# Performance work log

Hardware: AMD Instinct MI355X
Metric: run time of the kernel (lower is better)

Reference implementation:

```python
import jax, jax.numpy as jnp
import numpy as np

H = 1024
A = H // 2
B = 32
S = 1024
T = 1024


def setup_inputs() -> dict:
    key = jax.random.key(0)
    ks = jax.random.split(key, 16)
    sc = 0.02
    inp = {
        "hidden": jax.random.normal(ks[0], (1, B, H), jnp.float32),
        "encoder_hiddens": jax.random.normal(ks[1], (S, B, H), jnp.float32),
        "h0_s": jax.random.normal(ks[2], (T, B, H), jnp.float32),
        "ax": jax.random.uniform(ks[3], (B, S, 1), jnp.float32),
        # weights: torch Linear(in,out,bias=False) -> W has shape [out,in], y = x @ W.T
        "W1": jax.random.normal(ks[4], (A, H), jnp.float32) * sc,
        "W2": jax.random.normal(ks[5], (A, H), jnp.float32) * sc,
        "W3": jax.random.normal(ks[6], (A, 1), jnp.float32) * sc,
        "W4": jax.random.normal(ks[7], (1, 3 * A), jnp.float32) * sc,
        "W5": jax.random.normal(ks[8], (A, H), jnp.float32) * sc,
        "W6": jax.random.normal(ks[9], (A, H), jnp.float32) * sc,
        "W7": jax.random.normal(ks[10], (A, H), jnp.float32) * sc,
        "W8": jax.random.normal(ks[11], (1, 3 * A), jnp.float32) * sc,
        "W9": jax.random.normal(ks[12], (H, H), jnp.float32) * sc,
        "W10": jax.random.normal(ks[13], (H, H), jnp.float32) * sc,
        "W11": jax.random.normal(ks[14], (1, 2 * H), jnp.float32) * sc,
    }
    return inp


def reference(hidden, encoder_hiddens, h0_s, ax,
              W1, W2, W3, W4, W5, W6, W7, W8, W9, W10, W11):
    h = hidden[0]  # [B,H], hidden.squeeze(0)

    # ---- encoder (x) attention with coverage, vectorized over S ----
    wx = jnp.einsum('sbh,ah->sba', encoder_hiddens, W1)          # [S,B,A]
    wxy = h @ W2.T                                               # [B,A]
    # Linear3 on ax[:, j] ([B,1]): outer product with W3 column
    wxr = ax[:, :, 0][:, :, None] * W3[:, 0][None, None, :]       # [B,S,A]
    wxr = jnp.transpose(wxr, (1, 0, 2))                           # [S,B,A]
    cat_x = jnp.tanh(jnp.concatenate(
        [wx, jnp.broadcast_to(wxy, (S,) + wxy.shape), wxr], axis=-1))  # [S,B,3A]
    exi = jnp.einsum('sbc,oc->bso', cat_x, W4)                    # [B,S,1]
    axi = jax.nn.softmax(exi, axis=1)                             # [B,S,1]
    cxi = jnp.einsum('bs,sbh->bh', axi[:, :, 0], encoder_hiddens)  # [B,H]
    ax_new = ax + axi

    # ---- decoder-history (t) attention, vectorized over T ----
    wt = jnp.einsum('tbh,ah->tba', h0_s, W5)                      # [T,B,A]
    wtx = cxi @ W6.T                                              # [B,A]
    wty = h @ W7.T                                                # [B,A]
    Tn = h0_s.shape[0]
    cat_t = jnp.tanh(jnp.concatenate(
        [wt,
         jnp.broadcast_to(wtx, (Tn,) + wtx.shape),
         jnp.broadcast_to(wty, (Tn,) + wty.shape)], axis=-1))     # [T,B,3A]
    eti = jnp.einsum('tbc,oc->bto', cat_t, W8)                    # [B,T,1]
    ati = jax.nn.softmax(eti, axis=1)
    cti = jnp.einsum('bt,tbh->bh', ati[:, :, 0], h0_s)            # [B,H]

    # ---- gated fusion ----
    gxi = jnp.tanh(cxi @ W9.T)
    gti = jnp.tanh(cti @ W10.T)
    zi = jax.nn.sigmoid(jnp.concatenate([cxi, cti], axis=1) @ W11.T)  # [B,1]
    ci = zi * gxi + (1.0 - zi) * gti                              # [B,H]
    return ci, ax_new
```

## Files before the change

### kernel.cpp

```cpp
#include <hip/hip_runtime.h>
#include <hip/hip_bf16.h>

#define HH 1024
#define AA 512
#define BB 32
#define SS 1024
#define TN 1024
#define M_ENC (SS*BB)
#define M_TOT ((SS+TN)*BB)
#define NCH 8

typedef __attribute__((ext_vector_type(8))) short short8;
typedef __attribute__((ext_vector_type(4))) float f4;

union bfu { __hip_bfloat16 h; unsigned short u; };
__device__ __forceinline__ unsigned short f2b(float x) {
  bfu t; t.h = __float2bfloat16(x); return t.u;
}
__device__ __forceinline__ float tanh_fast(float x) {
  float e = __expf(2.f * x);
  return 1.f - 2.f / (e + 1.f);
}

__global__ void wprep(const float* __restrict__ W, unsigned short* __restrict__ Wc) {
  const int t = blockIdx.x * 256 + threadIdx.x;
  const int lane = t & 63;
  const int rg = (t >> 6) & 31;
  const int kb = t >> 11;
  const int row = rg * 16 + (lane & 15);
  const int k = kb * 32 + ((lane >> 4) << 3);
  const float* src = W + (size_t)row * HH + k;
  f4 v0 = *(const f4*)(src);
  f4 v1 = *(const f4*)(src + 4);
  short8 o;
  o[0] = f2b(v0[0]); o[1] = f2b(v0[1]); o[2] = f2b(v0[2]); o[3] = f2b(v0[3]);
  o[4] = f2b(v1[0]); o[5] = f2b(v1[1]); o[6] = f2b(v1[2]); o[7] = f2b(v1[3]);
  *(short8*)(Wc + (size_t)t * 8) = o;
}

__global__ __launch_bounds__(1024, 4)
void e1_gemm(const float* __restrict__ enc, const float* __restrict__ h0,
             const unsigned short* __restrict__ W1c, const unsigned short* __restrict__ W5c,
             const float* __restrict__ W4, const float* __restrict__ W8,
             float* __restrict__ e1) {
  const int wg   = blockIdx.x;
  const int tid  = threadIdx.x;
  const int lane = tid & 63;
  const int wave = tid >> 6;
  const int rowg = wave >> 3;
  const int colg = wave & 7;
  const int l15  = lane & 15;
  const int lg   = lane >> 4;

  const bool is_enc = (wg * 128) < M_ENC;
  const float* __restrict__ Xg = is_enc ? enc : h0;
  const unsigned short* __restrict__ Wc = is_enc ? W1c : W5c;
  const float* __restrict__ Vg = is_enc ? W4 : W8;
  const int row0 = is_enc ? wg * 128 : wg * 128 - M_ENC;

  __shared__ char lds_raw[2 * 49152 + 4096];
  float* lred = (float*)(lds_raw + 2 * 49152);

  float vvv[4];
#pragma unroll
  for (int cf = 0; cf < 4; ++cf) vvv[cf] = Vg[colg * 64 + cf * 16 + l15];

  f4 acc[4][4];
#pragma unroll
  for (int i = 0; i < 4; ++i)
#pragma unroll
    for (int j = 0; j < 4; ++j) acc[i][j] = (f4){0.f, 0.f, 0.f, 0.f};

#define STAGE(buf, kb_) do {                                                  \
    const int kbase_ = (kb_) * 32;                                            \
    const int arow_ = tid >> 3;                                               \
    const int sl_ = tid & 7;                                                  \
    const int sg_ = sl_ ^ (arow_ & 7);                                        \
    const float* gA_ = Xg + (size_t)(row0 + arow_) * HH + kbase_ + sg_ * 4;   \
    char* lA_ = lds_raw + (buf) * 49152 + tid * 16;                           \
    __builtin_amdgcn_global_load_lds(                                         \
        (const __attribute__((address_space(1))) void*)gA_,                   \
        (__attribute__((address_space(3))) void*)lA_, 16, 0, 0);              \
    _Pragma("unroll")                                                         \
    for (int p_ = 0; p_ < 2; ++p_) {                                          \
      const int idx_ = p_ * 1024 + tid;                                       \
      const char* gB_ = (const char*)Wc + (size_t)(kb_) * 32768 + idx_ * 16;  \
      char* lB_ = lds_raw + (buf) * 49152 + 16384 + idx_ * 16;                \
      __builtin_amdgcn_global_load_lds(                                       \
          (const __attribute__((address_space(1))) void*)gB_,                 \
          (__attribute__((address_space(3))) void*)lB_, 16, 0, 0);            \
    }                                                                         \
  } while (0)

  STAGE(0, 0);
  __syncthreads();

  int cur = 0;
#pragma unroll 1
  for (int kb = 0; kb < 32; ++kb) {
    if (kb < 31) STAGE(cur ^ 1, kb + 1);

    const char* Ab = lds_raw + cur * 49152;
    const char* Bb = Ab + 16384;

    short8 bfr[4];
#pragma unroll
    for (int cf = 0; cf < 4; ++cf)
      bfr[cf] = *(const short8*)(Bb + (((colg * 4 + cf) * 64 + lane) * 16));

#pragma unroll
    for (int rt = 0; rt < 4; ++rt) {
      const int row = rowg * 64 + rt * 16 + l15;
      const int x = row & 7;
      f4 a0 = *(const f4*)(Ab + row * 128 + (((lg * 2)     ^ x) * 16));
      f4 a1 = *(const f4*)(Ab + row * 128 + (((lg * 2 + 1) ^ x) * 16));
      short8 af;
      af[0] = f2b(a0[0]); af[1] = f2b(a0[1]); af[2] = f2b(a0[2]); af[3] = f2b(a0[3]);
      af[4] = f2b(a1[0]); af[5] = f2b(a1[1]); af[6] = f2b(a1[2]); af[7] = f2b(a1[3]);
#pragma unroll
      for (int cf = 0; cf < 4; ++cf)
        acc[rt][cf] = __builtin_amdgcn_mfma_f32_16x16x32_bf16(af, bfr[cf], acc[rt][cf], 0, 0, 0);
    }
    __syncthreads();
    cur ^= 1;
  }
#undef STAGE

#pragma unroll
  for (int rt = 0; rt < 4; ++rt) {
    float ps[4] = {0.f, 0.f, 0.f, 0.f};
#pragma unroll
    for (int cf = 0; cf < 4; ++cf) {
      const float w = vvv[cf];
#pragma unroll
      for (int r = 0; r < 4; ++r) ps[r] += w * tanh_fast(acc[rt][cf][r]);
    }
#pragma unroll
    for (int r = 0; r < 4; ++r) {
#pragma unroll
      for (int off = 1; off < 16; off <<= 1) ps[r] += __shfl_xor(ps[r], off);
    }
    if (l15 == 0) {
#pragma unroll
      for (int r = 0; r < 4; ++r)
        lred[colg * 128 + rowg * 64 + rt * 16 + lg * 4 + r] = ps[r];
    }
  }
  __syncthreads();
  if (tid < 128) {
    float s = 0.f;
#pragma unroll
    for (int c = 0; c < 8; ++c) s += lred[c * 128 + tid];
    e1[(size_t)wg * 128 + tid] = s;
  }
}

__global__ void exf_kernel(const float* __restrict__ e1, const float* __restrict__ ax,
                           const float* __restrict__ W3, const float* __restrict__ W4,
                           float* __restrict__ exf) {
  __shared__ float w3s[AA], w4r[AA];
  const int tid = threadIdx.x;
  for (int i = tid; i < AA; i += 256) { w3s[i] = W3[i]; w4r[i] = W4[2 * AA + i]; }
  __syncthreads();
  const int b = blockIdx.x >> 2;
  const int s = (blockIdx.x & 3) * 256 + tid;
  const float x = ax[b * SS + s];
  float er = 0.f;
#pragma unroll 8
  for (int a = 0; a < AA; ++a) er += w4r[a] * tanh_fast(x * w3s[a]);
  exf[b * SS + s] = e1[s * BB + b] + er;
}

__global__ void softmax_bs(const float* __restrict__ ein, const float* __restrict__ ax,
                           float* __restrict__ wout, float* __restrict__ axnew) {
  const int b = blockIdx.x, tid = threadIdx.x;
  __shared__ float red[256];
  float loc[4];
  float m = -1e30f;
#pragma unroll
  for (int i = 0; i < 4; ++i) { loc[i] = ein[b * SS + i * 256 + tid]; m = fmaxf(m, loc[i]); }
  red[tid] = m; __syncthreads();
  for (int off = 128; off > 0; off >>= 1) {
    if (tid < off) red[tid] = fmaxf(red[tid], red[tid + off]);
    __syncthreads();
  }
  m = red[0]; __syncthreads();
  float sum = 0.f;
#pragma unroll
  for (int i = 0; i < 4; ++i) { loc[i] = __expf(loc[i] - m); sum += loc[i]; }
  red[tid] = sum; __syncthreads();
  for (int off = 128; off > 0; off >>= 1) {
    if (tid < off) red[tid] += red[tid + off];
    __syncthreads();
  }
  const float inv = 1.f / red[0];
#pragma unroll
  for (int i = 0; i < 4; ++i) {
    const int s = i * 256 + tid;
    const float a_ = loc[i] * inv;
    wout[b * SS + s] = a_;
    axnew[b * SS + s] = ax[b * SS + s] + a_;
  }
}

__global__ void softmax_tb(const float* __restrict__ ein, float* __restrict__ wout) {
  const int b = blockIdx.x, tid = threadIdx.x;
  __shared__ float red[256];
  float loc[4];
  float m = -1e30f;
#pragma unroll
  for (int i = 0; i < 4; ++i) { loc[i] = ein[(i * 256 + tid) * BB + b]; m = fmaxf(m, loc[i]); }
  red[tid] = m; __syncthreads();
  for (int off = 128; off > 0; off >>= 1) {
    if (tid < off) red[tid] = fmaxf(red[tid], red[tid + off]);
    __syncthreads();
  }
  m = red[0]; __syncthreads();
  float sum = 0.f;
#pragma unroll
  for (int i = 0; i < 4; ++i) { loc[i] = __expf(loc[i] - m); sum += loc[i]; }
  red[tid] = sum; __syncthreads();
  for (int off = 128; off > 0; off >>= 1) {
    if (tid < off) red[tid] += red[tid + off];
    __syncthreads();
  }
  const float inv = 1.f / red[0];
#pragma unroll
  for (int i = 0; i < 4; ++i) wout[b * TN + (i * 256 + tid)] = loc[i] * inv;
}

__global__ void wpart(const float* __restrict__ X, const float* __restrict__ w,
                      float* __restrict__ part) {
  const int b = blockIdx.x / NCH, ch = blockIdx.x % NCH;
  const int tid = threadIdx.x;
  __shared__ float ws[SS / NCH];
  if (tid < SS / NCH) ws[tid] = w[b * SS + ch * (SS / NCH) + tid];
  __syncthreads();
  f4 acc = (f4){0.f, 0.f, 0.f, 0.f};
  const float* base = X + ((size_t)(ch * (SS / NCH)) * BB + b) * HH + tid * 4;
  for (int i = 0; i < SS / NCH; ++i) {
    f4 x = *(const f4*)(base + (size_t)i * BB * HH);
    acc += ws[i] * x;
  }
  *(f4*)&part[((size_t)(b * NCH + ch)) * HH + tid * 4] = acc;
}

__global__ void wreduce(const float* __restrict__ part, float* __restrict__ out) {
  const int idx = blockIdx.x * 256 + threadIdx.x;
  const int b = idx / HH, h = idx % HH;
  float s = 0.f;
#pragma unroll
  for (int ch = 0; ch < NCH; ++ch) s += part[((size_t)(b * NCH + ch)) * HH + h];
  out[idx] = s;
}

__global__ void zi_kernel(const float* __restrict__ cxi, const float* __restrict__ cti,
                          const float* __restrict__ W11, float* __restrict__ zi) {
  const int b = blockIdx.x, tid = threadIdx.x;
  float s = 0.f;
  for (int i = tid; i < HH; i += 256) s += cxi[b * HH + i] * W11[i] + cti[b * HH + i] * W11[HH + i];
  __shared__ float red[4];
  for (int off = 32; off > 0; off >>= 1) s += __shfl_down(s, off);
  if ((tid & 63) == 0) red[tid >> 6] = s;
  __syncthreads();
  if (tid == 0) {
    float t = red[0] + red[1] + red[2] + red[3];
    zi[b] = 1.f / (1.f + __expf(-t));
  }
}

__global__ void ci_kernel(const float* __restrict__ cxi, const float* __restrict__ cti,
                          const float* __restrict__ W9, const float* __restrict__ W10,
                          const float* __restrict__ zi, float* __restrict__ out_ci) {
  const int b = blockIdx.x >> 2, hb = blockIdx.x & 3, tid = threadIdx.x;
  const int h = hb * 256 + tid;
  __shared__ float cx[HH], ct[HH];
  for (int i = tid; i < HH; i += 256) { cx[i] = cxi[b * HH + i]; ct[i] = cti[b * HH + i]; }
  __syncthreads();
  const float* __restrict__ w9r  = W9  + (size_t)h * HH;
  const float* __restrict__ w10r = W10 + (size_t)h * HH;
  float gx = 0.f, gt = 0.f;
  for (int k = 0; k < HH; k += 4) {
    f4 a = *(const f4*)(w9r + k);
    f4 c = *(const f4*)(w10r + k);
    gx += cx[k] * a[0] + cx[k + 1] * a[1] + cx[k + 2] * a[2] + cx[k + 3] * a[3];
    gt += ct[k] * c[0] + ct[k + 1] * c[1] + ct[k + 2] * c[2] + ct[k + 3] * c[3];
  }
  const float z = zi[b];
  out_ci[b * HH + h] = z * tanhf(gx) + (1.f - z) * tanhf(gt);
}

extern "C" void kernel_launch(void* const* d_in, const int* in_sizes, int n_in,
                              void* d_out, int out_size, void* d_ws, size_t ws_size,
                              hipStream_t stream) {
  const float* enc = (const float*)d_in[1];
  const float* h0  = (const float*)d_in[2];
  const float* ax  = (const float*)d_in[3];
  const float* W1  = (const float*)d_in[4];
  const float* W3  = (const float*)d_in[6];
  const float* W4  = (const float*)d_in[7];
  const float* W5  = (const float*)d_in[8];
  const float* W8  = (const float*)d_in[11];
  const float* W9  = (const float*)d_in[12];
  const float* W10 = (const float*)d_in[13];
  const float* W11 = (const float*)d_in[14];
  float* out = (float*)d_out;

  float* w = (float*)d_ws;
  unsigned short* W1c = (unsigned short*)w;
  unsigned short* W5c = (unsigned short*)(w + 262144);
  float* partx = w;
  float* partt = w + 262144;
  float* e1    = w + 524288;
  float* exf   = w + 589824;
  float* axi   = w + 622592;
  float* ati   = w + 655360;
  float* cxi   = w + 688128;
  float* cti   = w + 720896;
  float* zi    = w + 753664;

  wprep<<<256, 256, 0, stream>>>(W1, W1c);
  wprep<<<256, 256, 0, stream>>>(W5, W5c);
  e1_gemm<<<M_TOT / 128, 1024, 0, stream>>>(enc, h0, W1c, W5c, W4, W8, e1);
  exf_kernel<<<BB * 4, 256, 0, stream>>>(e1, ax, W3, W4, exf);
  softmax_bs<<<BB, 256, 0, stream>>>(exf, ax, axi, out + BB * HH);
  softmax_tb<<<BB, 256, 0, stream>>>(e1 + M_ENC, ati);
  wpart<<<BB * NCH, 256, 0, stream>>>(enc, axi, partx);
  wpart<<<BB * NCH, 256, 0, stream>>>(h0, ati, partt);
  wreduce<<<BB * HH / 256, 256, 0, stream>>>(partx, cxi);
  wreduce<<<BB * HH / 256, 256, 0, stream>>>(partt, cti);
  zi_kernel<<<BB, 256, 0, stream>>>(cxi, cti, W11, zi);
  ci_kernel<<<BB * 4, 256, 0, stream>>>(cxi, cti, W9, W10, zi, out);
}
```

Baseline: 256.4 us.

## Convert A tile to bf16 once on load instead of per MFMA read

The GEMM's fp32 A tile used to be copied straight into LDS with global_load_lds, and every wave converted it to bf16 on each read. Now half the threads load A into registers, convert it to bf16 once, and write a swizzled bf16 tile into LDS after the MFMA loop. This halves the A footprint in LDS (from 96KB+ down to 80KB total) and removes redundant conversions. The trade-off is register-staged loads instead of async direct-to-LDS copies. The weighted-sum loop in wpart is also unrolled by 4.

```diff
diff --git a/kernel.cpp b/kernel.cpp
--- a/kernel.cpp
+++ b/kernel.cpp
@@ -58,8 +58,8 @@
   const float* __restrict__ Vg = is_enc ? W4 : W8;
   const int row0 = is_enc ? wg * 128 : wg * 128 - M_ENC;
 
-  __shared__ char lds_raw[2 * 49152 + 4096];
-  float* lred = (float*)(lds_raw + 2 * 49152);
+  __shared__ char lds_raw[2 * 40960];
+  float* lred = (float*)lds_raw;
 
   float vvv[4];
 #pragma unroll
@@ -71,60 +71,75 @@
 #pragma unroll
     for (int j = 0; j < 4; ++j) acc[i][j] = (f4){0.f, 0.f, 0.f, 0.f};
 
-#define STAGE(buf, kb_) do {                                                  \
-    const int kbase_ = (kb_) * 32;                                            \
-    const int arow_ = tid >> 3;                                               \
-    const int sl_ = tid & 7;                                                  \
-    const int sg_ = sl_ ^ (arow_ & 7);                                        \
-    const float* gA_ = Xg + (size_t)(row0 + arow_) * HH + kbase_ + sg_ * 4;   \
-    char* lA_ = lds_raw + (buf) * 49152 + tid * 16;                           \
-    __builtin_amdgcn_global_load_lds(                                         \
-        (const __attribute__((address_space(1))) void*)gA_,                   \
-        (__attribute__((address_space(3))) void*)lA_, 16, 0, 0);              \
+  const int arow  = tid >> 2;
+  const int kslot = tid & 3;
+  const int acol  = kslot ^ ((arow >> 1) & 3);
+  const float* aSrc = Xg + (size_t)(row0 + arow) * HH + kslot * 8;
+  const int aDst = arow * 64 + acol * 16;
+
+  const int aRd = (rowg * 64 + l15) * 64 + ((lg ^ ((l15 >> 1) & 3)) << 4);
+  const int bRd = colg * 4096 + lane * 16;
+
+#define BGLL(buf, kb_) do {                                                   \
     _Pragma("unroll")                                                         \
     for (int p_ = 0; p_ < 2; ++p_) {                                          \
       const int idx_ = p_ * 1024 + tid;                                       \
       const char* gB_ = (const char*)Wc + (size_t)(kb_) * 32768 + idx_ * 16;  \
-      char* lB_ = lds_raw + (buf) * 49152 + 16384 + idx_ * 16;                \
+      char* lB_ = lds_raw + (buf) * 40960 + 8192 + idx_ * 16;                 \
       __builtin_amdgcn_global_load_lds(                                       \
           (const __attribute__((address_space(1))) void*)gB_,                 \
           (__attribute__((address_space(3))) void*)lB_, 16, 0, 0);            \
     }                                                                         \
   } while (0)
 
-  STAGE(0, 0);
+#define AWRITE(buf, v0_, v1_) do {                                            \
+    short8 o_;                                                                \
+    o_[0] = f2b(v0_[0]); o_[1] = f2b(v0_[1]);                                 \
+    o_[2] = f2b(v0_[2]); o_[3] = f2b(v0_[3]);                                 \
+    o_[4] = f2b(v1_[0]); o_[5] = f2b(v1_[1]);                                 \
+    o_[6] = f2b(v1_[2]); o_[7] = f2b(v1_[3]);                                 \
+    *(short8*)(lds_raw + (buf) * 40960 + aDst) = o_;                          \
+  } while (0)
+
+  f4 a0n, a1n;
+  if (tid < 512) { a0n = *(const f4*)(aSrc); a1n = *(const f4*)(aSrc + 4); }
+  BGLL(0, 0);
+  if (tid < 512) AWRITE(0, a0n, a1n);
   __syncthreads();
 
   int cur = 0;
 #pragma unroll 1
   for (int kb = 0; kb < 32; ++kb) {
-    if (kb < 31) STAGE(cur ^ 1, kb + 1);
-
-    const char* Ab = lds_raw + cur * 49152;
-    const char* Bb = Ab + 16384;
+    if (kb < 31) {
+      if (tid < 512) {
+        a0n = *(const f4*)(aSrc + (kb + 1) * 32);
+        a1n = *(const f4*)(aSrc + (kb + 1) * 32 + 4);
+      }
+      BGLL(cur ^ 1, kb + 1);
+    }
+
+    const char* Ab = lds_raw + cur * 40960;
+    const char* Bb = Ab + 8192;
 
     short8 bfr[4];
 #pragma unroll
     for (int cf = 0; cf < 4; ++cf)
-      bfr[cf] = *(const short8*)(Bb + (((colg * 4 + cf) * 64 + lane) * 16));
+      bfr[cf] = *(const short8*)(Bb + bRd + cf * 1024);
 
 #pragma unroll
     for (int rt = 0; rt < 4; ++rt) {
-      const int row = rowg * 64 + rt * 16 + l15;
-      const int x = row & 7;
-      f4 a0 = *(const f4*)(Ab + row * 128 + (((lg * 2)     ^ x) * 16));
-      f4 a1 = *(const f4*)(Ab + row * 128 + (((lg * 2 + 1) ^ x) * 16));
-      short8 af;
-      af[0] = f2b(a0[0]); af[1] = f2b(a0[1]); af[2] = f2b(a0[2]); af[3] = f2b(a0[3]);
-      af[4] = f2b(a1[0]); af[5] = f2b(a1[1]); af[6] = f2b(a1[2]); af[7] = f2b(a1[3]);
+      short8 af = *(const short8*)(Ab + aRd + rt * 1024);
 #pragma unroll
       for (int cf = 0; cf < 4; ++cf)
         acc[rt][cf] = __builtin_amdgcn_mfma_f32_16x16x32_bf16(af, bfr[cf], acc[rt][cf], 0, 0, 0);
     }
+
+    if (kb < 31 && tid < 512) AWRITE(cur ^ 1, a0n, a1n);
     __syncthreads();
     cur ^= 1;
   }
-#undef STAGE
+#undef BGLL
+#undef AWRITE
 
 #pragma unroll
   for (int rt = 0; rt < 4; ++rt) {
@@ -238,6 +253,7 @@
   __syncthreads();
   f4 acc = (f4){0.f, 0.f, 0.f, 0.f};
   const float* base = X + ((size_t)(ch * (SS / NCH)) * BB + b) * HH + tid * 4;
+#pragma unroll 4
   for (int i = 0; i < SS / NCH; ++i) {
     f4 x = *(const f4*)(base + (size_t)i * BB * HH);
     acc += ws[i] * x;
```

After: 242.3 us. 5.5% less time.
